# Kernel tuning notes

Measured on AMD Instinct MI355X. Metric: run time of the kernel, lower is better.

Reference implementation:

```python
import jax, jax.numpy as jnp
import numpy as np

T, N = 20, 32768          # seq_length, numNodes
D_IN, D_EMB, D_H, D_OUT = 2, 64, 128, 5


def setup_inputs() -> dict:
    key = jax.random.key(0)
    ks = jax.random.split(key, 12)
    s = 0.05
    return {
        "nodes": jax.random.normal(ks[0], (T, N, D_IN), jnp.float32),
        "present_mask": jax.random.randint(ks[1], (T, N), 0, 2).astype(bool),
        "hidden_states": jax.random.normal(ks[2], (N, D_H), jnp.float32),
        "cell_states": jax.random.normal(ks[3], (N, D_H), jnp.float32),
        "W_embed": jax.random.normal(ks[4], (D_IN, D_EMB), jnp.float32) * s,
        "b_embed": jnp.zeros((D_EMB,), jnp.float32),
        "W_ih": jax.random.normal(ks[5], (D_EMB, 4 * D_H), jnp.float32) * s,
        "b_ih": jnp.zeros((4 * D_H,), jnp.float32),
        "W_hh": jax.random.normal(ks[6], (D_H, 4 * D_H), jnp.float32) * s,
        "b_hh": jnp.zeros((4 * D_H,), jnp.float32),
        "W_out": jax.random.normal(ks[7], (D_H, D_OUT), jnp.float32) * s,
        "b_out": jnp.zeros((D_OUT,), jnp.float32),
    }


def reference(nodes, present_mask, hidden_states, cell_states,
              W_embed, b_embed, W_ih, b_ih, W_hh, b_hh, W_out, b_out):
    # Per-frame: gather present nodes -> embed+ReLU (dropout=eval identity)
    # -> LSTMCell -> scatter h/c/output back. Gather+scatter is expressed as
    # a masked update, which is mathematically identical.
    def step(carry, frame):
        h, c = carry
        x, mask = frame                      # x: [N,2], mask: [N]
        emb = jax.nn.relu(x @ W_embed + b_embed)              # [N,Demb]
        gates = emb @ W_ih + b_ih + h @ W_hh + b_hh           # [N,4H]
        i, f, g, o = jnp.split(gates, 4, axis=-1)             # torch order
        i, f, o = jax.nn.sigmoid(i), jax.nn.sigmoid(f), jax.nn.sigmoid(o)
        g = jnp.tanh(g)
        c_new = f * c + i * g
        h_new = o * jnp.tanh(c_new)
        m = mask[:, None]
        h = jnp.where(m, h_new, h)
        c = jnp.where(m, c_new, c)
        out = jnp.where(m, h_new @ W_out + b_out, 0.0)        # absent -> zeros
        return (h, c), out

    (h_fin, c_fin), outputs = jax.lax.scan(
        step, (hidden_states, cell_states), (nodes, present_mask))
    return outputs, h_fin, c_fin                              # [T,N,5],[N,H],[N,H]
```

## Files before the change

### kernel.cpp

```cpp
#include <hip/hip_runtime.h>
#include <cstddef>


typedef __attribute__((ext_vector_type(8))) short  s16x8;
typedef __attribute__((ext_vector_type(4))) float  f32x4;

namespace {
constexpr int T_STEPS = 20;
constexpr int NN      = 32768;
constexpr int D_EMB   = 64;
constexpr int D_H     = 128;
constexpr int D_OUT   = 5;
constexpr int G4      = 512;
constexpr int MT      = 64;
constexpr int BLOCK   = 512;
constexpr int GRID    = NN / MT;
constexpr int WP_ELEMS   = 8 * 4 * 6 * 64 * 8;
constexpr int WOUT_ELEMS = 4 * 64 * 8;
constexpr int A_ELEMS    = 24 * 64 * 8;
constexpr float LOG2E = 1.4426950408889634f;
constexpr float AM4   = -4.0f * LOG2E;
constexpr float AP2   =  2.0f * LOG2E;
constexpr float CINV  = 0.34657359027997264f;
constexpr size_t OFF_H = (size_t)T_STEPS * NN * D_OUT;
constexpr size_t OFF_C = OFF_H + (size_t)NN * D_H;
}

__device__ __forceinline__ unsigned short f2bf(float x) {
    unsigned u = __float_as_uint(x);
    u = (u + 0x7FFFu + ((u >> 16) & 1u)) >> 16;
    return (unsigned short)u;
}
__device__ __forceinline__ unsigned short f2bf_hw(float x) {
    __bf16 b = (__bf16)x;
    union { __bf16 b; unsigned short u; } cv;
    cv.b = b;
    return cv.u;
}
__device__ __forceinline__ float bf2f(unsigned short h) {
    return __uint_as_float(((unsigned)h) << 16);
}
__device__ __forceinline__ float exp2f_fast(float x) {
#if __has_builtin(__builtin_amdgcn_exp2f)
    return __builtin_amdgcn_exp2f(x);
#else
    return __expf(x * 0.6931471805599453f);
#endif
}
__device__ __forceinline__ float sig_pre(float a) {
    return __builtin_amdgcn_rcpf(1.0f + exp2f_fast(a));
}

__global__ void prepack_kernel(const float* __restrict__ W_ih,
                               const float* __restrict__ b_ih,
                               const float* __restrict__ W_hh,
                               const float* __restrict__ b_hh,
                               const float* __restrict__ W_out,
                               unsigned short* __restrict__ Wp,
                               unsigned short* __restrict__ WoutF,
                               float* __restrict__ b_sum) {
    int idx = blockIdx.x * blockDim.x + threadIdx.x;
    if (idx < WP_ELEMS) {
        int j    = idx & 7;
        int L    = (idx >> 3) & 63;
        int rest = idx >> 9;
        int kb   = rest % 6;
        int gw   = rest / 6;
        int g    = gw & 3, w = gw >> 2;
        int k    = kb * 32 + (L >> 4) * 8 + j;
        int col  = g * D_H + w * 16 + (L & 15);
        float v  = (k < D_EMB) ? W_ih[k * G4 + col] : W_hh[(k - D_EMB) * G4 + col];
        float s  = (g == 2) ? (2.0f * LOG2E) : (-LOG2E);
        Wp[idx] = f2bf(v * s);
    } else if (idx < WP_ELEMS + WOUT_ELEMS) {
        int i2 = idx - WP_ELEMS;
        int j = i2 & 7, L = (i2 >> 3) & 63, kb2 = i2 >> 9;
        int k = kb2 * 32 + (L >> 4) * 8 + j;
        int n = L & 15;
        WoutF[i2] = (n < D_OUT) ? f2bf(W_out[k * D_OUT + n]) : (unsigned short)0;
    }
    if (idx < G4) {
        int g = idx / D_H;
        float s = (g == 2) ? (2.0f * LOG2E) : (-LOG2E);
        b_sum[idx] = (b_ih[idx] + b_hh[idx]) * s;
    }
}

__global__ __launch_bounds__(BLOCK, 2) void vlstm_kernel(
    const float* __restrict__ nodes,
    const int*   __restrict__ mask,
    const float* __restrict__ h0,
    const float* __restrict__ c0,
    const float* __restrict__ W_embed,
    const float* __restrict__ b_embed,
    const float* __restrict__ b_out,
    const unsigned short* __restrict__ Wp,
    const unsigned short* __restrict__ WoutF,
    const float* __restrict__ b_sum,
    float* __restrict__ out)
{
    __shared__ __align__(16) unsigned short A[2][A_ELEMS];
    __shared__ __align__(16) float st_out[2][MT * D_OUT];
    __shared__ float We_s[2 * D_EMB];
    __shared__ float be_s[D_EMB];
    __shared__ unsigned long long msk64[2];

    const int tid  = threadIdx.x;
    const int wave = tid >> 6;
    const int L    = tid & 63;
    const int quad = L >> 4;
    const int l15  = L & 15;
    const int n_base = blockIdx.x * MT;

    const unsigned short* wbase = Wp + (size_t)wave * (4 * 6 * 64 * 8);
    s16x8 Bf[4][6];
    #pragma unroll
    for (int g = 0; g < 4; g++)
        #pragma unroll
        for (int kb = 0; kb < 6; kb++)
            Bf[g][kb] = *(const s16x8*)(wbase + ((g * 6 + kb) * 64 + L) * 8);
    s16x8 WoF[4];
    #pragma unroll
    for (int kb2 = 0; kb2 < 4; kb2++)
        WoF[kb2] = *(const s16x8*)(WoutF + ((kb2 * 64) + L) * 8);

    const int u_lane = wave * 16 + l15;
    f32x4 biasv[4];
    #pragma unroll
    for (int g = 0; g < 4; g++) {
        float b = b_sum[g * D_H + wave * 16 + l15];
        biasv[g] = (f32x4){b, b, b, b};
    }
    const float bo = (l15 < D_OUT) ? b_out[l15] : 0.0f;

    const int kb_u = 2 + (u_lane >> 5);
    const int fl   = ((u_lane >> 3) & 3) * 16 + quad * 4;
    const int j_u  = u_lane & 7;

    for (int i = tid; i < 3 * D_EMB; i += BLOCK) {
        if (i < 2 * D_EMB) We_s[i] = W_embed[i];
        else               be_s[i - 2 * D_EMB] = b_embed[i - 2 * D_EMB];
    }

    float          cL[4][4];
    unsigned short hr[4][4];
    #pragma unroll
    for (int rt = 0; rt < 4; rt++)
        #pragma unroll
        for (int r = 0; r < 4; r++) {
            int m = rt * 16 + quad * 4 + r;
            cL[rt][r] = AP2 * c0[(size_t)(n_base + m) * D_H + u_lane];
            hr[rt][r] = f2bf_hw(h0[(size_t)(n_base + m) * D_H + u_lane]);
            A[0][((rt * 6 + kb_u) * 64 + fl + r) * 8 + j_u] = hr[rt][r];
        }

    const int node_e = tid >> 3;
    const int eb     = tid & 7;
    const int idx_e  = (((node_e >> 4) * 6 + (eb >> 2)) * 64 + (eb & 3) * 16 + (node_e & 15)) * 8;
    {
        const float2* xp = (const float2*)(nodes + ((size_t)0 * NN + n_base + node_e) * 2);
        float2 x = *xp;
        s16x8 ev;
        #pragma unroll
        for (int j = 0; j < 8; j++) {
            int e = eb * 8 + j;
            float v = fmaf(x.x, We_s[e], fmaf(x.y, We_s[D_EMB + e], be_s[e]));
            ev[j] = (short)f2bf_hw(fmaxf(v, 0.0f));
        }
        *(s16x8*)(&A[0][idx_e]) = ev;
        if (wave == 0) {
            int lm0 = mask[n_base + L];
            unsigned long long bm0 = __ballot(lm0 != 0);
            if (L == 0) msk64[0] = bm0;
        }
    }
    __syncthreads();

#define GEMM_RT(rt) do {                                                       \
    {   s16x8 af0 = *(const s16x8*)(Ar + (((rt) * 6 + 0) * 64 + L) * 8);       \
        _Pragma("unroll")                                                      \
        for (int g = 0; g < 4; g++)                                            \
            acc[rt][g] = __builtin_amdgcn_mfma_f32_16x16x32_bf16(              \
                af0, Bf[g][0], biasv[g], 0, 0, 0); }                           \
    _Pragma("unroll")                                                          \
    for (int kb = 1; kb < 6; kb++) {                                           \
        s16x8 af = *(const s16x8*)(Ar + (((rt) * 6 + kb) * 64 + L) * 8);       \
        _Pragma("unroll")                                                      \
        for (int g = 0; g < 4; g++)                                            \
            acc[rt][g] = __builtin_amdgcn_mfma_f32_16x16x32_bf16(              \
                af, Bf[g][kb], acc[rt][g], 0, 0, 0); }                         \
} while (0)

#define ACT_RT(rt) do {                                                        \
    unsigned nib = (unsigned)(M >> ((rt) * 16 + quad * 4)) & 0xFu;             \
    _Pragma("unroll")                                                          \
    for (int r = 0; r < 4; r++) {                                              \
        float gi = sig_pre(acc[rt][0][r]);                                     \
        float gf = sig_pre(acc[rt][1][r]);                                     \
        float rg = sig_pre(acc[rt][2][r]);                                     \
        float go = sig_pre(acc[rt][3][r]);                                     \
        float ggL = fmaf(AM4, rg, AP2);                   \
        float cnL = fmaf(gf, cL[rt][r], gi * ggL);        \
        float rr  = __builtin_amdgcn_rcpf(1.0f + exp2f_fast(cnL));             \
        float hv  = go * fmaf(-2.0f, rr, 1.0f);           \
        unsigned short hb = f2bf_hw(hv);                                       \
        if ((nib >> r) & 1u) { cL[rt][r] = cnL; hr[rt][r] = hb; }              \
        Aw[(((rt) * 6 + kb_u) * 64 + fl + r) * 8 + j_u] = hr[rt][r];           \
    }                                                                          \
} while (0)

    for (int t = 0; t < T_STEPS; t++) {
        unsigned short* __restrict__ Ar = A[t & 1];
        unsigned short* __restrict__ Aw = A[(t + 1) & 1];

        float2 xv = make_float2(0.0f, 0.0f);
        int    lm = 0;
        if (t + 1 < T_STEPS) {
            xv = *(const float2*)(nodes + ((size_t)(t + 1) * NN + n_base + node_e) * 2);
            if (wave == 0) lm = mask[(size_t)(t + 1) * NN + n_base + L];
        }
        const unsigned long long M = msk64[t & 1];

        f32x4 acc[4][4];
        GEMM_RT(0);
        GEMM_RT(1);
        GEMM_RT(2);
        ACT_RT(0);
        GEMM_RT(3);
        ACT_RT(1);

        if (t + 1 < T_STEPS) {
            s16x8 ev;
            #pragma unroll
            for (int j = 0; j < 8; j++) {
                int e = eb * 8 + j;
                float v = fmaf(xv.x, We_s[e], fmaf(xv.y, We_s[D_EMB + e], be_s[e]));
                ev[j] = (short)f2bf_hw(fmaxf(v, 0.0f));
            }
            *(s16x8*)(Aw + idx_e) = ev;
            if (wave == 0) {
                unsigned long long bm = __ballot(lm != 0);
                if (L == 0) msk64[(t + 1) & 1] = bm;
            }
        }

        ACT_RT(2);
        ACT_RT(3);

        __syncthreads();

        if (t > 0 && wave >= 4) {
            int j = tid - 256;
            if (j < MT * D_OUT / 4)
                ((f32x4*)(out + ((size_t)(t - 1) * NN + n_base) * D_OUT))[j] =
                    ((const f32x4*)st_out[(t - 1) & 1])[j];
        }

        if (wave < 4) {
            f32x4 ao = (f32x4){0.0f, 0.0f, 0.0f, 0.0f};
            #pragma unroll
            for (int kb2 = 0; kb2 < 4; kb2++) {
                s16x8 af = *(const s16x8*)(Aw + ((wave * 6 + 2 + kb2) * 64 + L) * 8);
                ao = __builtin_amdgcn_mfma_f32_16x16x32_bf16(af, WoF[kb2], ao, 0, 0, 0);
            }
            if (l15 < D_OUT) {
                unsigned nib_o = (unsigned)(M >> (wave * 16 + quad * 4)) & 0xFu;
                #pragma unroll
                for (int r = 0; r < 4; r++) {
                    int node = wave * 16 + quad * 4 + r;
                    st_out[t & 1][node * D_OUT + l15] =
                        ((nib_o >> r) & 1u) ? (ao[r] + bo) : 0.0f;
                }
            }
        }
    }
#undef GEMM_RT
#undef ACT_RT

    __syncthreads();
    if (tid < MT * D_OUT / 4)
        ((f32x4*)(out + ((size_t)(T_STEPS - 1) * NN + n_base) * D_OUT))[tid] =
            ((const f32x4*)st_out[(T_STEPS - 1) & 1])[tid];

    for (int i = tid; i < MT * D_H; i += BLOCK) {
        int node = i >> 7, u = i & 127;
        int k = D_EMB + u;
        int idx = (((node >> 4) * 6 + (k >> 5)) * 64 + ((k >> 3) & 3) * 16 + (node & 15)) * 8 + (k & 7);
        out[OFF_H + (size_t)(n_base + node) * D_H + u] = bf2f(A[0][idx]);
    }

    __syncthreads();
    float* cs = (float*)A;
    #pragma unroll
    for (int rt = 0; rt < 4; rt++)
        #pragma unroll
        for (int r = 0; r < 4; r++) {
            int m = rt * 16 + quad * 4 + r;
            cs[m * 129 + u_lane] = CINV * cL[rt][r];
        }
    __syncthreads();
    for (int i = tid; i < MT * D_H; i += BLOCK) {
        int node = i >> 7, u = i & 127;
        out[OFF_C + (size_t)(n_base + node) * D_H + u] = cs[node * 129 + u];
    }
}

extern "C" void kernel_launch(void* const* d_in, const int* in_sizes, int n_in,
                              void* d_out, int out_size, void* d_ws, size_t ws_size,
                              hipStream_t stream) {
    const float* nodes   = (const float*)d_in[0];
    const int*   mask    = (const int*)  d_in[1];
    const float* h0      = (const float*)d_in[2];
    const float* c0      = (const float*)d_in[3];
    const float* W_embed = (const float*)d_in[4];
    const float* b_embed = (const float*)d_in[5];
    const float* W_ih    = (const float*)d_in[6];
    const float* b_ih    = (const float*)d_in[7];
    const float* W_hh    = (const float*)d_in[8];
    const float* b_hh    = (const float*)d_in[9];
    const float* W_out   = (const float*)d_in[10];
    const float* b_out   = (const float*)d_in[11];
    float* out = (float*)d_out;

    unsigned short* Wp    = (unsigned short*)d_ws;
    unsigned short* WoutF = Wp + WP_ELEMS;
    float*          b_sum = (float*)(WoutF + WOUT_ELEMS);

    prepack_kernel<<<(WP_ELEMS + WOUT_ELEMS + 255) / 256, 256, 0, stream>>>(
        W_ih, b_ih, W_hh, b_hh, W_out, Wp, WoutF, b_sum);

    vlstm_kernel<<<GRID, BLOCK, 0, stream>>>(
        nodes, mask, h0, c0, W_embed, b_embed, b_out, Wp, WoutF, b_sum, out);
}
```

Baseline: 274.3 us.

## Double node tile per block and pipeline output projection into next timestep

Each block now handles 128 nodes instead of 64, so the grid is half as large. The recurrent GEMM and the activations are interleaved over eight row tiles, using a two-slot accumulator to cut register pressure. The bias is added after the MFMA instead of being used as its accumulator init. The output projection for step t-1 now runs inside step t, spread across all waves, with W_out staged in LDS and results written straight to global memory instead of through a shared staging buffer. The aim is to amortise per-block weight loading and hide the projection and its stores behind the main GEMM. The cost is fewer resident blocks per CU and longer serial work per block.

```diff
diff --git a/kernel.cpp b/kernel.cpp
--- a/kernel.cpp
+++ b/kernel.cpp
@@ -12,12 +12,13 @@
 constexpr int D_H     = 128;
 constexpr int D_OUT   = 5;
 constexpr int G4      = 512;
-constexpr int MT      = 64;
+constexpr int MT      = 128;
 constexpr int BLOCK   = 512;
 constexpr int GRID    = NN / MT;
+constexpr int RT_N    = MT / 16;
 constexpr int WP_ELEMS   = 8 * 4 * 6 * 64 * 8;
 constexpr int WOUT_ELEMS = 4 * 64 * 8;
-constexpr int A_ELEMS    = 24 * 64 * 8;
+constexpr int A_ELEMS    = RT_N * 6 * 64 * 8;
 constexpr float LOG2E = 1.4426950408889634f;
 constexpr float AM4   = -4.0f * LOG2E;
 constexpr float AP2   =  2.0f * LOG2E;
@@ -100,10 +101,10 @@
     float* __restrict__ out)
 {
     __shared__ __align__(16) unsigned short A[2][A_ELEMS];
-    __shared__ __align__(16) float st_out[2][MT * D_OUT];
+    __shared__ __align__(16) unsigned short WoS[WOUT_ELEMS];
     __shared__ float We_s[2 * D_EMB];
     __shared__ float be_s[D_EMB];
-    __shared__ unsigned long long msk64[2];
+    __shared__ __align__(16) unsigned long long msk64[2][2];
 
     const int tid  = threadIdx.x;
     const int wave = tid >> 6;
@@ -119,18 +120,11 @@
         #pragma unroll
         for (int kb = 0; kb < 6; kb++)
             Bf[g][kb] = *(const s16x8*)(wbase + ((g * 6 + kb) * 64 + L) * 8);
-    s16x8 WoF[4];
-    #pragma unroll
-    for (int kb2 = 0; kb2 < 4; kb2++)
-        WoF[kb2] = *(const s16x8*)(WoutF + ((kb2 * 64) + L) * 8);
 
     const int u_lane = wave * 16 + l15;
-    f32x4 biasv[4];
-    #pragma unroll
-    for (int g = 0; g < 4; g++) {
-        float b = b_sum[g * D_H + wave * 16 + l15];
-        biasv[g] = (f32x4){b, b, b, b};
-    }
+    float bias[4];
+    #pragma unroll
+    for (int g = 0; g < 4; g++) bias[g] = b_sum[g * D_H + u_lane];
     const float bo = (l15 < D_OUT) ? b_out[l15] : 0.0f;
 
     const int kb_u = 2 + (u_lane >> 5);
@@ -141,11 +135,12 @@
         if (i < 2 * D_EMB) We_s[i] = W_embed[i];
         else               be_s[i - 2 * D_EMB] = b_embed[i - 2 * D_EMB];
     }
-
-    float          cL[4][4];
-    unsigned short hr[4][4];
-    #pragma unroll
-    for (int rt = 0; rt < 4; rt++)
+    for (int i = tid; i < WOUT_ELEMS; i += BLOCK) WoS[i] = WoutF[i];
+
+    float          cL[RT_N][4];
+    unsigned short hr[RT_N][4];
+    #pragma unroll
+    for (int rt = 0; rt < RT_N; rt++)
         #pragma unroll
         for (int r = 0; r < 4; r++) {
             int m = rt * 16 + quad * 4 + r;
@@ -154,24 +149,36 @@
             A[0][((rt * 6 + kb_u) * 64 + fl + r) * 8 + j_u] = hr[rt][r];
         }
 
-    const int node_e = tid >> 3;
-    const int eb     = tid & 7;
-    const int idx_e  = (((node_e >> 4) * 6 + (eb >> 2)) * 64 + (eb & 3) * 16 + (node_e & 15)) * 8;
+    const int node_e = tid >> 2;
+    const int eb2    = tid & 3;
+    int idx_e[2];
+    #pragma unroll
+    for (int s = 0; s < 2; s++) {
+        int e0 = eb2 * 16 + s * 8;
+        idx_e[s] = (((node_e >> 4) * 6 + (e0 >> 5)) * 64 +
+                    ((e0 >> 3) & 3) * 16 + (node_e & 15)) * 8;
+    }
+
+#define EMB_WRITE(AW, XV) do {                                                 \
+    _Pragma("unroll")                                                          \
+    for (int s = 0; s < 2; s++) {                                              \
+        s16x8 ev;                                                              \
+        _Pragma("unroll")                                                      \
+        for (int j = 0; j < 8; j++) {                                          \
+            int e = eb2 * 16 + s * 8 + j;                                      \
+            float v = fmaf((XV).x, We_s[e], fmaf((XV).y, We_s[D_EMB + e], be_s[e])); \
+            ev[j] = (short)f2bf_hw(fmaxf(v, 0.0f));                            \
+        }                                                                      \
+        *(s16x8*)((AW) + idx_e[s]) = ev;                                       \
+    } } while (0)
+
     {
-        const float2* xp = (const float2*)(nodes + ((size_t)0 * NN + n_base + node_e) * 2);
-        float2 x = *xp;
-        s16x8 ev;
-        #pragma unroll
-        for (int j = 0; j < 8; j++) {
-            int e = eb * 8 + j;
-            float v = fmaf(x.x, We_s[e], fmaf(x.y, We_s[D_EMB + e], be_s[e]));
-            ev[j] = (short)f2bf_hw(fmaxf(v, 0.0f));
-        }
-        *(s16x8*)(&A[0][idx_e]) = ev;
-        if (wave == 0) {
-            int lm0 = mask[n_base + L];
-            unsigned long long bm0 = __ballot(lm0 != 0);
-            if (L == 0) msk64[0] = bm0;
+        float2 x0 = *(const float2*)(nodes + (size_t)(n_base + node_e) * 2);
+        EMB_WRITE(A[0], x0);
+        int lm0 = (tid < MT) ? mask[n_base + tid] : 0;
+        if (wave < 2) {
+            unsigned long long bm = __ballot(lm0 != 0);
+            if (L == 0) msk64[0][wave] = bm;
         }
     }
     __syncthreads();
@@ -180,25 +187,25 @@
     {   s16x8 af0 = *(const s16x8*)(Ar + (((rt) * 6 + 0) * 64 + L) * 8);       \
         _Pragma("unroll")                                                      \
         for (int g = 0; g < 4; g++)                                            \
-            acc[rt][g] = __builtin_amdgcn_mfma_f32_16x16x32_bf16(              \
-                af0, Bf[g][0], biasv[g], 0, 0, 0); }                           \
+            acc[(rt) & 1][g] = __builtin_amdgcn_mfma_f32_16x16x32_bf16(        \
+                af0, Bf[g][0], (f32x4){0.f, 0.f, 0.f, 0.f}, 0, 0, 0); }        \
     _Pragma("unroll")                                                          \
     for (int kb = 1; kb < 6; kb++) {                                           \
         s16x8 af = *(const s16x8*)(Ar + (((rt) * 6 + kb) * 64 + L) * 8);       \
         _Pragma("unroll")                                                      \
         for (int g = 0; g < 4; g++)                                            \
-            acc[rt][g] = __builtin_amdgcn_mfma_f32_16x16x32_bf16(              \
-                af, Bf[g][kb], acc[rt][g], 0, 0, 0); }                         \
+            acc[(rt) & 1][g] = __builtin_amdgcn_mfma_f32_16x16x32_bf16(        \
+                af, Bf[g][kb], acc[(rt) & 1][g], 0, 0, 0); }                   \
 } while (0)
 
-#define ACT_RT(rt) do {                                                        \
-    unsigned nib = (unsigned)(M >> ((rt) * 16 + quad * 4)) & 0xFu;             \
+#define ACT_RT(rt, MW) do {                                                    \
+    unsigned nib = (unsigned)((MW) >> (((rt) & 3) * 16 + quad * 4)) & 0xFu;    \
     _Pragma("unroll")                                                          \
     for (int r = 0; r < 4; r++) {                                              \
-        float gi = sig_pre(acc[rt][0][r]);                                     \
-        float gf = sig_pre(acc[rt][1][r]);                                     \
-        float rg = sig_pre(acc[rt][2][r]);                                     \
-        float go = sig_pre(acc[rt][3][r]);                                     \
+        float gi = sig_pre(acc[(rt) & 1][0][r] + bias[0]);                     \
+        float gf = sig_pre(acc[(rt) & 1][1][r] + bias[1]);                     \
+        float rg = sig_pre(acc[(rt) & 1][2][r] + bias[2]);                     \
+        float go = sig_pre(acc[(rt) & 1][3][r] + bias[3]);                     \
         float ggL = fmaf(AM4, rg, AP2);                   \
         float cnL = fmaf(gf, cL[rt][r], gi * ggL);        \
         float rr  = __builtin_amdgcn_rcpf(1.0f + exp2f_fast(cnL));             \
@@ -206,93 +213,86 @@
         unsigned short hb = f2bf_hw(hv);                                       \
         if ((nib >> r) & 1u) { cL[rt][r] = cnL; hr[rt][r] = hb; }              \
         Aw[(((rt) * 6 + kb_u) * 64 + fl + r) * 8 + j_u] = hr[rt][r];           \
+    } } while (0)
+
+#define OPROJ(ARP, TIDX, MPA, MPB) do {                                        \
+    f32x4 ao = (f32x4){0.f, 0.f, 0.f, 0.f};                                    \
+    _Pragma("unroll")                                                          \
+    for (int kb2 = 0; kb2 < 4; kb2++) {                                        \
+        s16x8 af = *(const s16x8*)((ARP) + ((wave * 6 + 2 + kb2) * 64 + L) * 8); \
+        s16x8 wf = *(const s16x8*)(WoS + (kb2 * 64 + L) * 8);                  \
+        ao = __builtin_amdgcn_mfma_f32_16x16x32_bf16(af, wf, ao, 0, 0, 0);     \
     }                                                                          \
-} while (0)
+    if (l15 < D_OUT) {                                                         \
+        unsigned long long Mw = (wave < 4) ? (MPA) : (MPB);                    \
+        unsigned nib = (unsigned)(Mw >> ((wave & 3) * 16 + quad * 4)) & 0xFu;  \
+        float* ob = out + ((size_t)(TIDX) * NN + n_base) * D_OUT + l15;        \
+        _Pragma("unroll")                                                      \
+        for (int r = 0; r < 4; r++) {                                          \
+            int node = wave * 16 + quad * 4 + r;                               \
+            ob[node * D_OUT] = ((nib >> r) & 1u) ? (ao[r] + bo) : 0.0f;        \
+        }                                                                      \
+    } } while (0)
+
+    unsigned long long Mp0 = 0, Mp1 = 0;
 
     for (int t = 0; t < T_STEPS; t++) {
         unsigned short* __restrict__ Ar = A[t & 1];
         unsigned short* __restrict__ Aw = A[(t + 1) & 1];
+
+        const unsigned long long M0 = msk64[t & 1][0];
+        const unsigned long long M1 = msk64[t & 1][1];
 
         float2 xv = make_float2(0.0f, 0.0f);
         int    lm = 0;
         if (t + 1 < T_STEPS) {
             xv = *(const float2*)(nodes + ((size_t)(t + 1) * NN + n_base + node_e) * 2);
-            if (wave == 0) lm = mask[(size_t)(t + 1) * NN + n_base + L];
-        }
-        const unsigned long long M = msk64[t & 1];
-
-        f32x4 acc[4][4];
+            if (tid < MT) lm = mask[(size_t)(t + 1) * NN + n_base + tid];
+        }
+
+        f32x4 acc[2][4];
         GEMM_RT(0);
         GEMM_RT(1);
+        ACT_RT(0, M0);
         GEMM_RT(2);
-        ACT_RT(0);
+        ACT_RT(1, M0);
         GEMM_RT(3);
-        ACT_RT(1);
-
+        ACT_RT(2, M0);
+        if (t > 0) OPROJ(Ar, t - 1, Mp0, Mp1);
+        ACT_RT(3, M0);
+        GEMM_RT(4);
+        GEMM_RT(5);
+        ACT_RT(4, M1);
+        GEMM_RT(6);
+        ACT_RT(5, M1);
+        GEMM_RT(7);
+        ACT_RT(6, M1);
         if (t + 1 < T_STEPS) {
-            s16x8 ev;
-            #pragma unroll
-            for (int j = 0; j < 8; j++) {
-                int e = eb * 8 + j;
-                float v = fmaf(xv.x, We_s[e], fmaf(xv.y, We_s[D_EMB + e], be_s[e]));
-                ev[j] = (short)f2bf_hw(fmaxf(v, 0.0f));
+            EMB_WRITE(Aw, xv);
+            if (wave < 2) {
+                unsigned long long bm = __ballot(lm != 0);
+                if (L == 0) msk64[(t + 1) & 1][wave] = bm;
             }
-            *(s16x8*)(Aw + idx_e) = ev;
-            if (wave == 0) {
-                unsigned long long bm = __ballot(lm != 0);
-                if (L == 0) msk64[(t + 1) & 1] = bm;
-            }
-        }
-
-        ACT_RT(2);
-        ACT_RT(3);
-
+        }
+        ACT_RT(7, M1);
+
+        Mp0 = M0; Mp1 = M1;
         __syncthreads();
-
-        if (t > 0 && wave >= 4) {
-            int j = tid - 256;
-            if (j < MT * D_OUT / 4)
-                ((f32x4*)(out + ((size_t)(t - 1) * NN + n_base) * D_OUT))[j] =
-                    ((const f32x4*)st_out[(t - 1) & 1])[j];
-        }
-
-        if (wave < 4) {
-            f32x4 ao = (f32x4){0.0f, 0.0f, 0.0f, 0.0f};
-            #pragma unroll
-            for (int kb2 = 0; kb2 < 4; kb2++) {
-                s16x8 af = *(const s16x8*)(Aw + ((wave * 6 + 2 + kb2) * 64 + L) * 8);
-                ao = __builtin_amdgcn_mfma_f32_16x16x32_bf16(af, WoF[kb2], ao, 0, 0, 0);
-            }
-            if (l15 < D_OUT) {
-                unsigned nib_o = (unsigned)(M >> (wave * 16 + quad * 4)) & 0xFu;
-                #pragma unroll
-                for (int r = 0; r < 4; r++) {
-                    int node = wave * 16 + quad * 4 + r;
-                    st_out[t & 1][node * D_OUT + l15] =
-                        ((nib_o >> r) & 1u) ? (ao[r] + bo) : 0.0f;
-                }
-            }
-        }
-    }
-#undef GEMM_RT
-#undef ACT_RT
-
-    __syncthreads();
-    if (tid < MT * D_OUT / 4)
-        ((f32x4*)(out + ((size_t)(T_STEPS - 1) * NN + n_base) * D_OUT))[tid] =
-            ((const f32x4*)st_out[(T_STEPS - 1) & 1])[tid];
+    }
+
+    OPROJ(A[0], T_STEPS - 1, Mp0, Mp1);
 
     for (int i = tid; i < MT * D_H; i += BLOCK) {
         int node = i >> 7, u = i & 127;
-        int k = D_EMB + u;
-        int idx = (((node >> 4) * 6 + (k >> 5)) * 64 + ((k >> 3) & 3) * 16 + (node & 15)) * 8 + (k & 7);
+        int idx = (((node >> 4) * 6 + 2 + (u >> 5)) * 64 +
+                   ((u >> 3) & 3) * 16 + (node & 15)) * 8 + (u & 7);
         out[OFF_H + (size_t)(n_base + node) * D_H + u] = bf2f(A[0][idx]);
     }
 
     __syncthreads();
     float* cs = (float*)A;
     #pragma unroll
-    for (int rt = 0; rt < 4; rt++)
+    for (int rt = 0; rt < RT_N; rt++)
         #pragma unroll
         for (int r = 0; r < 4; r++) {
             int m = rt * 16 + quad * 4 + r;
@@ -303,6 +303,11 @@
         int node = i >> 7, u = i & 127;
         out[OFF_C + (size_t)(n_base + node) * D_H + u] = cs[node * 129 + u];
     }
+
+#undef EMB_WRITE
+#undef GEMM_RT
+#undef ACT_RT
+#undef OPROJ
 }
 
 extern "C" void kernel_launch(void* const* d_in, const int* in_sizes, int n_in,
```

Measured after the change: 279.9 us. 2.1% more time.
